# Performance work log

Hardware: AMD Instinct MI355X
Metric: run time of the kernel (lower is better)

Reference implementation:

```python
import jax, jax.numpy as jnp
import numpy as np


def _lstm_scan(x_bte, W_ih, W_hh, b_ih, b_hh, h0, c0):
    """Single-layer LSTM over time (torch gate order i,f,g,o).
    x_bte: [B,T,E]; returns (h_seq [B,T,H], (h_T, c_T))."""
    H = h0.shape[-1]
    # precompute input projections for all timesteps: [T,B,4H]
    xp = jnp.einsum('bte,ge->tbg', x_bte, W_ih) + (b_ih + b_hh)

    def step(carry, xg):
        h, c = carry
        gates = xg + h @ W_hh.T  # [B,4H]
        i, f, g, o = jnp.split(gates, 4, axis=-1)
        c = jax.nn.sigmoid(f) * c + jax.nn.sigmoid(i) * jnp.tanh(g)
        h = jax.nn.sigmoid(o) * jnp.tanh(c)
        return (h, c), h

    (hT, cT), h_seq = jax.lax.scan(step, (h0, c0), xp)
    return jnp.transpose(h_seq, (1, 0, 2)), (hT, cT)


def setup_inputs() -> dict:
    key = jax.random.key(0)
    ks = jax.random.split(key, 10)
    V, E, H = 32000, 256, 512
    B, S, T = 64, 64, 32
    s = 0.02
    return {
        'src': jax.random.randint(ks[0], (B, S), 0, V),
        'tgt': jax.random.randint(ks[1], (B, T), 0, V),
        'enc_emb': jax.random.normal(ks[2], (V, E), jnp.float32) * s,
        'dec_emb': jax.random.normal(ks[3], (V, E), jnp.float32) * s,
        'enc_Wih': jax.random.normal(ks[4], (4 * H, E), jnp.float32) * s,
        'enc_Whh': jax.random.normal(ks[5], (4 * H, H), jnp.float32) * s,
        'enc_bih': jnp.zeros((4 * H,), jnp.float32),
        'enc_bhh': jnp.zeros((4 * H,), jnp.float32),
        'dec_Wih': jax.random.normal(ks[6], (4 * H, E), jnp.float32) * s,
        'dec_Whh': jax.random.normal(ks[7], (4 * H, H), jnp.float32) * s,
        'dec_bih': jnp.zeros((4 * H,), jnp.float32),
        'dec_bhh': jnp.zeros((4 * H,), jnp.float32),
        'fc_W': jax.random.normal(ks[8], (V, H), jnp.float32) * s,
        'fc_b': jnp.zeros((V,), jnp.float32),
    }


def reference(src, tgt, enc_emb, dec_emb, enc_Wih, enc_Whh, enc_bih, enc_bhh,
              dec_Wih, dec_Whh, dec_bih, dec_bhh, fc_W, fc_b):
    B, T = tgt.shape
    H = enc_Whh.shape[-1]
    V = fc_W.shape[0]
    h0 = jnp.zeros((B, H), jnp.float32)
    c0 = jnp.zeros((B, H), jnp.float32)

    # Encoder (dropout=0.0 -> identity)
    emb_src = enc_emb[src]  # [B,S,E]
    _, (hT, cT) = _lstm_scan(emb_src, enc_Wih, enc_Whh, enc_bih, enc_bhh, h0, c0)
    hT = jax.lax.stop_gradient(hT)  # .detach() in torch source
    cT = jax.lax.stop_gradient(cT)

    # Decoder, teacher_forcing_ratio=1.0 -> inputs are tgt[:, :-1]
    emb_tgt = dec_emb[tgt[:, :-1]]  # [B,T-1,E]
    h_seq, _ = _lstm_scan(emb_tgt, dec_Wih, dec_Whh, dec_bih, dec_bhh, hT, cT)
    logits = jnp.einsum('bth,vh->btv', h_seq, fc_W) + fc_b  # [B,T-1,V]

    # outputs[:,0] stays zeros as in torch code
    outputs = jnp.concatenate([jnp.zeros((B, 1, V), jnp.float32), logits], axis=1)
    return outputs
```

## Files before the change

kernel.cpp:

```cpp
#include <hip/hip_runtime.h>
#include <cstdint>
#include <cstddef>

#define NB    64
#define SENC  64
#define TDEC  31
#define EDIM  256
#define HDIM  512
#define VOCAB 32000
#define MROWS (NB * TDEC)
#define MPAD  2048
#define NBLK  256

#define OFF_HTA  0
#define OFF_HTB  (OFF_HTA + HDIM * NB * 4)
#define OFF_XPE  (OFF_HTB + HDIM * NB * 4)
#define OFF_XPD  (OFF_XPE + 256 * SENC * 8 * NB * 4)
#define OFF_HS   (OFF_XPD + 256 * TDEC * 8 * NB * 4)
#define OFF_FCW  (OFF_HS + MPAD * HDIM * 2)

typedef __attribute__((ext_vector_type(8))) short bf16x8;
typedef __attribute__((ext_vector_type(4))) float f32x4;

__device__ __forceinline__ float sigf(float x) { return 1.0f / (1.0f + __expf(-x)); }
__device__ __forceinline__ float tanhfast(float x) {
  return 1.0f - 2.0f / (__expf(2.0f * x) + 1.0f);
}
__device__ __forceinline__ unsigned short f2bf(float x) {
  unsigned int u = __float_as_uint(x);
  u += 0x7fffu + ((u >> 16) & 1u);
  return (unsigned short)(u >> 16);
}
__device__ __forceinline__ unsigned pack2(float a, float b) {
  return (unsigned)f2bf(a) | ((unsigned)f2bf(b) << 16);
}

__global__ __launch_bounds__(256) void setup_k(const float* __restrict__ fc_W,
                                               unsigned short* __restrict__ fcw,
                                               float* __restrict__ hTA,
                                               unsigned short* __restrict__ hs,
                                               float* __restrict__ out) {
  const int gt = blockIdx.x * 256 + threadIdx.x;
  const int GSZ = 2048 * 256;
  const float4* s4 = (const float4*)fc_W;
  uint4* d4 = (uint4*)fcw;
  for (int i = gt; i < (VOCAB * HDIM / 8); i += GSZ) {
    float4 x = s4[2 * i], y = s4[2 * i + 1];
    uint4 v;
    v.x = pack2(x.x, x.y); v.y = pack2(x.z, x.w);
    v.z = pack2(y.x, y.y); v.w = pack2(y.z, y.w);
    d4[i] = v;
  }
  float4 z4 = make_float4(0.f, 0.f, 0.f, 0.f);
  for (int j = gt; j < NB * (VOCAB / 4); j += GSZ) {
    int b = j / (VOCAB / 4), q = j - b * (VOCAB / 4);
    ((float4*)out)[(size_t)b * (32 * (VOCAB / 4)) + q] = z4;
  }
  if (gt < HDIM * NB / 4) ((float4*)hTA)[gt] = z4;
  if (gt < (MPAD - MROWS) * HDIM / 8) {
    uint4 uz = {0u, 0u, 0u, 0u};
    ((uint4*)(hs + (size_t)MROWS * HDIM))[gt] = uz;
  }
}

__device__ void xp_phase(const int* idxmat, int istride, int S,
                         const float* emb, const float* Wih,
                         const float* bih, const float* bhh,
                         float* xp_out, int bid, int tid,
                         float* W_lds, float* pbuf, float* bias_lds) {
  const int lane = tid & 63;
  const int w = tid >> 6;
  {
    int r = tid >> 5;
    int e0 = (tid & 31) * 8;
    int row_g = (r >> 1) * HDIM + bid * 2 + (r & 1);
    const float* sp = Wih + (size_t)row_g * EDIM + e0;
    *(float4*)&W_lds[r * EDIM + e0]     = *(const float4*)sp;
    *(float4*)&W_lds[r * EDIM + e0 + 4] = *(const float4*)(sp + 4);
    if (tid < 8) {
      int rg = (tid >> 1) * HDIM + bid * 2 + (tid & 1);
      bias_lds[tid] = bih[rg] + bhh[rg];
    }
  }
  __syncthreads();
  for (int s = 0; s < S; ++s) {
    int idx = idxmat[lane * istride + s];
    const float* xrow = emb + (size_t)idx * EDIM;
    float acc[8];
#pragma unroll
    for (int r = 0; r < 8; ++r) acc[r] = 0.0f;
    for (int e = w * 64; e < w * 64 + 64; e += 4) {
      float4 xv = *(const float4*)&xrow[e];
#pragma unroll
      for (int r = 0; r < 8; ++r) {
        float4 wv = *(const float4*)&W_lds[r * EDIM + e];
        acc[r] += wv.x * xv.x + wv.y * xv.y + wv.z * xv.z + wv.w * xv.w;
      }
    }
#pragma unroll
    for (int r = 0; r < 8; ++r) pbuf[(w * 8 + r) * 64 + lane] = acc[r];
    __syncthreads();
    if (tid < 128) {
      int unit = tid >> 6, b = tid & 63;
#pragma unroll
      for (int gate = 0; gate < 4; ++gate) {
        int r = gate * 2 + unit;
        float v = bias_lds[r];
#pragma unroll
        for (int ww = 0; ww < 4; ++ww) v += pbuf[(ww * 8 + r) * 64 + b];
        xp_out[((size_t)(bid * S + s) * 8 + r) * 64 + b] = v;
      }
    }
    __syncthreads();
  }
}

struct XpParams {
  const int* src; const int* tgt;
  const float* enc_emb; const float* dec_emb;
  const float* enc_Wih; const float* enc_bih; const float* enc_bhh;
  const float* dec_Wih; const float* dec_bih; const float* dec_bhh;
  float* xpe; float* xpd;
};

__global__ __launch_bounds__(256) void xp_k(XpParams p) {
  __shared__ __align__(16) float W_lds[8 * EDIM];
  __shared__ float pbuf[32 * 64];
  __shared__ float bias_lds[8];
  const int bid = blockIdx.x;
  if (bid < 256)
    xp_phase(p.src, SENC, SENC, p.enc_emb, p.enc_Wih, p.enc_bih, p.enc_bhh,
             p.xpe, bid, threadIdx.x, W_lds, pbuf, bias_lds);
  else
    xp_phase(p.tgt, 32, TDEC, p.dec_emb, p.dec_Wih, p.dec_bih, p.dec_bhh,
             p.xpd, bid - 256, threadIdx.x, W_lds, pbuf, bias_lds);
}

__device__ __forceinline__ void grid_barrier(unsigned* flags, unsigned gen) {
  asm volatile("s_waitcnt vmcnt(0)" ::: "memory");
  __syncthreads();
  const int tid = threadIdx.x;
  if (tid == 0)
    __hip_atomic_store(&flags[blockIdx.x], gen, __ATOMIC_RELAXED,
                       __HIP_MEMORY_SCOPE_AGENT);
  if (tid < 64) {
    const unsigned* f4 = flags + tid * 4;
    for (;;) {
      unsigned a = __hip_atomic_load(&f4[0], __ATOMIC_RELAXED, __HIP_MEMORY_SCOPE_AGENT);
      unsigned b = __hip_atomic_load(&f4[1], __ATOMIC_RELAXED, __HIP_MEMORY_SCOPE_AGENT);
      unsigned c = __hip_atomic_load(&f4[2], __ATOMIC_RELAXED, __HIP_MEMORY_SCOPE_AGENT);
      unsigned d = __hip_atomic_load(&f4[3], __ATOMIC_RELAXED, __HIP_MEMORY_SCOPE_AGENT);
      unsigned m0 = a < b ? a : b;
      unsigned m1 = c < d ? c : d;
      unsigned m = m0 < m1 ? m0 : m1;
      if (__all((int)(m >= gen))) break;
      __builtin_amdgcn_s_sleep(1);
    }
    __builtin_amdgcn_fence(__ATOMIC_ACQUIRE, "agent");
  }
  __syncthreads();
}

__device__ void recur_phase(const float* Whh, const float* xp, int S, int gen0,
                            int last_phase, int bid, int tid,
                            float* W_lds, float* pbuf, float* c_lds,
                            float*& hp, float*& hn,
                            unsigned short* hs_or_null, unsigned* flags) {
  const int lane = tid & 63;
  const int w = tid >> 6;
  const int j0 = bid * 2;
  {
    int r = tid >> 5;
    int e0 = (tid & 31) * 16;
    int row_g = (r >> 1) * HDIM + j0 + (r & 1);
    const float* sp = Whh + (size_t)row_g * HDIM + e0;
#pragma unroll
    for (int q = 0; q < 4; ++q)
      *(float4*)&W_lds[r * HDIM + e0 + q * 4] = *(const float4*)(sp + q * 4);
  }
  __syncthreads();

  const int unit = tid >> 6;
  const int b = tid & 63;
  float xg[4];
  if (tid < 128) {
#pragma unroll
    for (int gate = 0; gate < 4; ++gate) {
      int r = gate * 2 + unit;
      xg[gate] = xp[((size_t)(bid * S) * 8 + r) * 64 + b];
    }
  }

  for (int s = 0; s < S; ++s) {
    const float* hpw = hp + (size_t)w * 128 * 64;
    float acc[8];
#pragma unroll
    for (int r = 0; r < 8; ++r) acc[r] = 0.0f;
    for (int kk = 0; kk < 128; kk += 4) {
      float h0 = hpw[(kk + 0) * 64 + lane];
      float h1 = hpw[(kk + 1) * 64 + lane];
      float h2 = hpw[(kk + 2) * 64 + lane];
      float h3 = hpw[(kk + 3) * 64 + lane];
#pragma unroll
      for (int r = 0; r < 8; ++r) {
        float4 wv = *(const float4*)&W_lds[r * HDIM + w * 128 + kk];
        acc[r] += wv.x * h0 + wv.y * h1 + wv.z * h2 + wv.w * h3;
      }
    }
#pragma unroll
    for (int r = 0; r < 8; ++r) pbuf[(w * 8 + r) * 64 + lane] = acc[r];
    __syncthreads();
    float xgn[4];
    if (tid < 128) {
      float g[4];
#pragma unroll
      for (int gate = 0; gate < 4; ++gate) {
        int r = gate * 2 + unit;
        float v = xg[gate];
#pragma unroll
        for (int ww = 0; ww < 4; ++ww) v += pbuf[(ww * 8 + r) * 64 + b];
        g[gate] = v;
      }
      float c = c_lds[unit * 64 + b];
      float iv = sigf(g[0]), fv = sigf(g[1]);
      float gv = tanhfast(g[2]), ov = sigf(g[3]);
      c = fv * c + iv * gv;
      float h = ov * tanhfast(c);
      c_lds[unit * 64 + b] = c;
      __hip_atomic_store(&hn[(j0 + unit) * 64 + b], h, __ATOMIC_RELAXED,
                         __HIP_MEMORY_SCOPE_AGENT);
      if (hs_or_null)
        hs_or_null[((size_t)b * TDEC + s) * HDIM + j0 + unit] = f2bf(h);
      int sn = (s + 1 < S) ? s + 1 : s;
#pragma unroll
      for (int gate = 0; gate < 4; ++gate) {
        int r = gate * 2 + unit;
        xgn[gate] = xp[((size_t)(bid * S + sn) * 8 + r) * 64 + b];
      }
    }
    if (!(last_phase && s == S - 1))
      grid_barrier(flags, (unsigned)(gen0 + s + 1));
    if (tid < 128) {
#pragma unroll
      for (int gate = 0; gate < 4; ++gate) xg[gate] = xgn[gate];
    }
    float* tmp = hp; hp = hn; hn = tmp;
  }
}

struct RecurParams {
  const float* enc_Whh; const float* dec_Whh;
  const float* xpe; const float* xpd;
  float* hTA; float* hTB;
  unsigned short* hs;
  unsigned* flags;
};

__global__ __launch_bounds__(256, 1) void recur_coop(RecurParams p) {
  __shared__ __align__(16) float W_lds[8 * HDIM];
  __shared__ float pbuf[32 * 64];
  __shared__ float c_lds[2 * 64];
  const int tid = threadIdx.x;
  const int bid = blockIdx.x;
  if (tid < 128) c_lds[tid] = 0.0f;
  __syncthreads();
  float* hp = p.hTA;
  float* hn = p.hTB;
  recur_phase(p.enc_Whh, p.xpe, SENC, 0, 0, bid, tid, W_lds, pbuf, c_lds,
              hp, hn, nullptr, p.flags);
  recur_phase(p.dec_Whh, p.xpd, TDEC, SENC, 1, bid, tid, W_lds, pbuf, c_lds,
              hp, hn, p.hs, p.flags);
}

__global__ __launch_bounds__(256) void fc_gemm(const unsigned short* __restrict__ A,
                                               const unsigned short* __restrict__ Bm,
                                               const float* __restrict__ bias,
                                               float* __restrict__ out) {
  __shared__ __align__(16) unsigned short As[128 * 32];
  __shared__ __align__(16) unsigned short Bs[128 * 32];
  const int tid = threadIdx.x;
  const int lane = tid & 63;
  const int w = tid >> 6;
  const int m0 = blockIdx.y * 128;
  const int n0 = blockIdx.x * 128;
  const int wm = (w >> 1) * 64;
  const int wn = (w & 1) * 64;
  const int ml = lane & 15;
  const int kq = (lane >> 4) * 8;

  f32x4 acc[4][4] = {};

  for (int k0 = 0; k0 < HDIM; k0 += 32) {
    for (int c = tid; c < 512; c += 256) {
      int row = c >> 2;
      int ko = (c & 3) * 8;
      *(uint4*)&As[c * 8] = *(const uint4*)(A + (size_t)(m0 + row) * HDIM + k0 + ko);
      *(uint4*)&Bs[c * 8] = *(const uint4*)(Bm + (size_t)(n0 + row) * HDIM + k0 + ko);
    }
    __syncthreads();
    bf16x8 fa[4], fb[4];
#pragma unroll
    for (int i = 0; i < 4; ++i)
      fa[i] = *(const bf16x8*)&As[(wm + 16 * i + ml) * 32 + kq];
#pragma unroll
    for (int j = 0; j < 4; ++j)
      fb[j] = *(const bf16x8*)&Bs[(wn + 16 * j + ml) * 32 + kq];
#pragma unroll
    for (int i = 0; i < 4; ++i)
#pragma unroll
      for (int j = 0; j < 4; ++j)
        acc[i][j] = __builtin_amdgcn_mfma_f32_16x16x32_bf16(fa[i], fb[j], acc[i][j], 0, 0, 0);
    __syncthreads();
  }

  const int rq = (lane >> 4) * 4;
#pragma unroll
  for (int j = 0; j < 4; ++j) {
    int n = n0 + wn + 16 * j + ml;
    float bv = bias[n];
#pragma unroll
    for (int i = 0; i < 4; ++i) {
#pragma unroll
      for (int r = 0; r < 4; ++r) {
        int m = m0 + wm + 16 * i + rq + r;
        if (m < MROWS) {
          int b = m / TDEC;
          int t = m - b * TDEC;
          out[((size_t)(b * 32 + t + 1)) * VOCAB + n] = acc[i][j][r] + bv;
        }
      }
    }
  }
}

extern "C" void kernel_launch(void* const* d_in, const int* in_sizes, int n_in,
                              void* d_out, int out_size, void* d_ws, size_t ws_size,
                              hipStream_t stream) {
  (void)in_sizes; (void)n_in; (void)out_size; (void)ws_size;
  const int* src      = (const int*)d_in[0];
  const int* tgt      = (const int*)d_in[1];
  const float* enc_emb = (const float*)d_in[2];
  const float* dec_emb = (const float*)d_in[3];
  const float* enc_Wih = (const float*)d_in[4];
  const float* enc_Whh = (const float*)d_in[5];
  const float* enc_bih = (const float*)d_in[6];
  const float* enc_bhh = (const float*)d_in[7];
  const float* dec_Wih = (const float*)d_in[8];
  const float* dec_Whh = (const float*)d_in[9];
  const float* dec_bih = (const float*)d_in[10];
  const float* dec_bhh = (const float*)d_in[11];
  const float* fc_W    = (const float*)d_in[12];
  const float* fc_b    = (const float*)d_in[13];
  char* ws = (char*)d_ws;
  float* hTA = (float*)(ws + OFF_HTA);
  float* hTB = (float*)(ws + OFF_HTB);
  float* xpe = (float*)(ws + OFF_XPE);
  float* xpd = (float*)(ws + OFF_XPD);
  unsigned short* hs  = (unsigned short*)(ws + OFF_HS);
  unsigned short* fcw = (unsigned short*)(ws + OFF_FCW);
  unsigned* flags = (unsigned*)(ws + OFF_HS + (size_t)MROWS * HDIM * 2);
  float* out = (float*)d_out;

  hipLaunchKernelGGL(setup_k, dim3(2048), dim3(256), 0, stream, fc_W, fcw, hTA, hs, out);

  XpParams xq = { src, tgt, enc_emb, dec_emb, enc_Wih, enc_bih, enc_bhh,
                  dec_Wih, dec_bih, dec_bhh, xpe, xpd };
  hipLaunchKernelGGL(xp_k, dim3(512), dim3(256), 0, stream, xq);

  RecurParams rp = { enc_Whh, dec_Whh, xpe, xpd, hTA, hTB, hs, flags };
  void* args[] = { &rp };
  hipLaunchCooperativeKernel((const void*)recur_coop, dim3(NBLK), dim3(256), args, 0, stream);

  hipLaunchKernelGGL(fc_gemm, dim3(VOCAB / 128, MPAD / 128), dim3(256), 0, stream,
                     hs, fcw, fc_b, out);
}
```

Measured before the change: 2.575 ms.

## Split recurrent matvec across 8 waves, read W_hh via scalar loads

The recurrent kernel now runs 512 threads per block, so each of 8 waves handles a 64-wide slice of the hidden dimension instead of 128. The slice of h is preloaded into registers. W_hh rows are read directly from global memory through wave-uniform pointers (readfirstlane), which allows scalar loads instead of staging the weights in LDS. The aim is to shorten the per-step critical path between grid barriers, at the cost of re-reading weights from cache every step, higher register pressure, and a larger partial-sum reduction.

Result: no change. 2.555 ms (-0.8%).

```diff
diff --git a/kernel.cpp b/kernel.cpp
--- a/kernel.cpp
+++ b/kernel.cpp
@@ -161,24 +161,21 @@
   __syncthreads();
 }
 
-__device__ void recur_phase(const float* Whh, const float* xp, int S, int gen0,
-                            int last_phase, int bid, int tid,
-                            float* W_lds, float* pbuf, float* c_lds,
+#define KW 64
+
+__device__ __forceinline__ void recur_phase(const float* Whh, const float* xp,
+                            int S, int gen0, int last_phase, int bid, int tid,
+                            float* pbuf, float* c_lds,
                             float*& hp, float*& hn,
                             unsigned short* hs_or_null, unsigned* flags) {
   const int lane = tid & 63;
-  const int w = tid >> 6;
+  const int wu = __builtin_amdgcn_readfirstlane(tid >> 6);
   const int j0 = bid * 2;
-  {
-    int r = tid >> 5;
-    int e0 = (tid & 31) * 16;
-    int row_g = (r >> 1) * HDIM + j0 + (r & 1);
-    const float* sp = Whh + (size_t)row_g * HDIM + e0;
-#pragma unroll
-    for (int q = 0; q < 4; ++q)
-      *(float4*)&W_lds[r * HDIM + e0 + q * 4] = *(const float4*)(sp + q * 4);
-  }
-  __syncthreads();
+
+  const float* Wr[8];
+#pragma unroll
+  for (int r = 0; r < 8; ++r)
+    Wr[r] = Whh + (size_t)((r >> 1) * HDIM + j0 + (r & 1)) * HDIM + wu * KW;
 
   const int unit = tid >> 6;
   const int b = tid & 63;
@@ -192,24 +189,23 @@
   }
 
   for (int s = 0; s < S; ++s) {
-    const float* hpw = hp + (size_t)w * 128 * 64;
+    float hreg[KW];
+    const float* hb = hp + (size_t)wu * KW * 64 + lane;
+#pragma unroll
+    for (int k = 0; k < KW; ++k) hreg[k] = hb[k * 64];
+
     float acc[8];
 #pragma unroll
     for (int r = 0; r < 8; ++r) acc[r] = 0.0f;
-    for (int kk = 0; kk < 128; kk += 4) {
-      float h0 = hpw[(kk + 0) * 64 + lane];
-      float h1 = hpw[(kk + 1) * 64 + lane];
-      float h2 = hpw[(kk + 2) * 64 + lane];
-      float h3 = hpw[(kk + 3) * 64 + lane];
-#pragma unroll
-      for (int r = 0; r < 8; ++r) {
-        float4 wv = *(const float4*)&W_lds[r * HDIM + w * 128 + kk];
-        acc[r] += wv.x * h0 + wv.y * h1 + wv.z * h2 + wv.w * h3;
-      }
-    }
-#pragma unroll
-    for (int r = 0; r < 8; ++r) pbuf[(w * 8 + r) * 64 + lane] = acc[r];
-    __syncthreads();
+#pragma unroll
+    for (int k = 0; k < KW; ++k) {
+#pragma unroll
+      for (int r = 0; r < 8; ++r) acc[r] += Wr[r][k] * hreg[k];
+    }
+#pragma unroll
+    for (int r = 0; r < 8; ++r) pbuf[(wu * 8 + r) * 64 + lane] = acc[r];
+    __syncthreads();
+
     float xgn[4];
     if (tid < 128) {
       float g[4];
@@ -218,7 +214,7 @@
         int r = gate * 2 + unit;
         float v = xg[gate];
 #pragma unroll
-        for (int ww = 0; ww < 4; ++ww) v += pbuf[(ww * 8 + r) * 64 + b];
+        for (int ww = 0; ww < 8; ++ww) v += pbuf[(ww * 8 + r) * 64 + b];
         g[gate] = v;
       }
       float c = c_lds[unit * 64 + b];
@@ -256,9 +252,8 @@
   unsigned* flags;
 };
 
-__global__ __launch_bounds__(256, 1) void recur_coop(RecurParams p) {
-  __shared__ __align__(16) float W_lds[8 * HDIM];
-  __shared__ float pbuf[32 * 64];
+__global__ __launch_bounds__(512, 2) void recur_coop(RecurParams p) {
+  __shared__ float pbuf[64 * 64];
   __shared__ float c_lds[2 * 64];
   const int tid = threadIdx.x;
   const int bid = blockIdx.x;
@@ -266,9 +261,9 @@
   __syncthreads();
   float* hp = p.hTA;
   float* hn = p.hTB;
-  recur_phase(p.enc_Whh, p.xpe, SENC, 0, 0, bid, tid, W_lds, pbuf, c_lds,
+  recur_phase(p.enc_Whh, p.xpe, SENC, 0, 0, bid, tid, pbuf, c_lds,
               hp, hn, nullptr, p.flags);
-  recur_phase(p.dec_Whh, p.xpd, TDEC, SENC, 1, bid, tid, W_lds, pbuf, c_lds,
+  recur_phase(p.dec_Whh, p.xpd, TDEC, SENC, 1, bid, tid, pbuf, c_lds,
               hp, hn, p.hs, p.flags);
 }
 
@@ -369,7 +364,7 @@
 
   RecurParams rp = { enc_Whh, dec_Whh, xpe, xpd, hTA, hTB, hs, flags };
   void* args[] = { &rp };
-  hipLaunchCooperativeKernel((const void*)recur_coop, dim3(NBLK), dim3(256), args, 0, stream);
+  hipLaunchCooperativeKernel((const void*)recur_coop, dim3(NBLK), dim3(512), args, 0, stream);
 
   hipLaunchKernelGGL(fc_gemm, dim3(VOCAB / 128, MPAD / 128), dim3(256), 0, stream,
                      hs, fcw, fc_b, out);
```
